# Kernel optimization log

Hardware: AMD Instinct MI355X
Metric: run time of the kernel (lower is better)

The kernel has to match this reference:

```python
import jax, jax.numpy as jnp
import numpy as np

N = 100000   # nodes
E = 1600000  # edges
IN = 128
H = 128
OUT = 128
G = 1000     # graphs


def setup_inputs() -> dict:
    key = jax.random.key(0)
    ks = jax.random.split(key, 6)
    x = jax.random.normal(ks[0], (N, IN), jnp.float32)
    edge_index = jax.random.randint(ks[1], (2, E), 0, N, dtype=jnp.int64)
    batch = jnp.sort(jax.random.randint(ks[2], (N,), 0, G, dtype=jnp.int64))
    # Glorot-ish init for the two GCN linear transforms
    W1 = jax.random.normal(ks[3], (IN, H), jnp.float32) * (1.0 / np.sqrt(IN))
    b1 = jnp.zeros((H,), jnp.float32)
    W2 = jax.random.normal(ks[4], (H, OUT), jnp.float32) * (1.0 / np.sqrt(H))
    b2 = jnp.zeros((OUT,), jnp.float32)
    return {"x": x, "edge_index": edge_index, "batch": batch,
            "W1": W1, "b1": b1, "W2": W2, "b2": b2, "num_graphs": G}


def reference(x, edge_index, batch, W1, b1, W2, b2, num_graphs):
    n = x.shape[0]
    src, dst = edge_index[0], edge_index[1]
    # GCN normalization with self-loops: deg includes the self-loop (+1)
    deg = jax.ops.segment_sum(jnp.ones(src.shape[0], x.dtype), dst,
                              num_segments=n) + 1.0
    dinv = jax.lax.rsqrt(deg)                 # [N]
    norm = dinv[src] * dinv[dst]              # [E] per-edge coefficient
    self_norm = dinv * dinv                   # [N] self-loop coefficient

    def gcn_conv(h, W, b):
        hw = h @ W                                            # [N, F] dense transform
        msg = norm[:, None] * hw[src]                         # gather + scale, [E, F]
        agg = jax.ops.segment_sum(msg, dst, num_segments=n)   # scatter-add
        return agg + self_norm[:, None] * hw + b              # self-loop + bias

    h = jax.nn.relu(gcn_conv(x, W1, b1))
    h = gcn_conv(h, W2, b2)

    # global_mean_pool over graph ids
    sums = jax.ops.segment_sum(h, batch, num_segments=num_graphs)
    counts = jax.ops.segment_sum(jnp.ones(n, h.dtype), batch,
                                 num_segments=num_graphs)
    return sums / jnp.maximum(counts, 1.0)[:, None]
```

## Files before the change

kernel.cpp:

```cpp
#include <hip/hip_runtime.h>
#include <hip/hip_fp16.h>

#define FDIM 128
#define BROWS 64
#define KCH 16
#define NCH (FDIM / KCH)
#define BSHIFT 9
#define BNODES 512
#define EPB 4096


__global__ __launch_bounds__(256) void bucket_count(const int* __restrict__ dst,
                                                    int* __restrict__ bcnt, int E) {
    __shared__ int lc[256];
    lc[threadIdx.x] = 0;
    __syncthreads();
    for (int e = blockIdx.x * blockDim.x + threadIdx.x; e < E;
         e += gridDim.x * blockDim.x)
        atomicAdd(&lc[dst[e] >> BSHIFT], 1);
    __syncthreads();
    int c = lc[threadIdx.x];
    if (c) atomicAdd(&bcnt[threadIdx.x], c);
}

__global__ void bucket_scan(const int* __restrict__ bcnt, int* __restrict__ bbase,
                            int* __restrict__ bcur, int* __restrict__ rp,
                            int E, int n, int nbuck) {
    __shared__ int s[2][256];
    int t = threadIdx.x;
    int v = (t < nbuck) ? bcnt[t] : 0;
    s[0][t] = v;
    __syncthreads();
    int cur = 0;
    for (int off = 1; off < 256; off <<= 1) {
        int x = s[cur][t];
        if (t >= off) x += s[cur][t - off];
        s[cur ^ 1][t] = x;
        cur ^= 1;
        __syncthreads();
    }
    int ex = s[cur][t] - v;
    if (t < nbuck) { bbase[t] = ex; bcur[t] = ex; }
    if (t == 0) { bbase[nbuck] = E; rp[n] = E; }
}

__global__ __launch_bounds__(256) void binscatter(const int* __restrict__ src,
                                                  const int* __restrict__ dst,
                                                  int* __restrict__ bcur,
                                                  unsigned* __restrict__ ebp, int E) {
    __shared__ int lcnt[256];
    __shared__ int gb[256];
    const int t = threadIdx.x;
    const int e0 = blockIdx.x * EPB;
    const int e1 = min(e0 + EPB, E);
    lcnt[t] = 0;
    __syncthreads();
    for (int e = e0 + t; e < e1; e += 256)
        atomicAdd(&lcnt[dst[e] >> BSHIFT], 1);
    __syncthreads();
    int c = lcnt[t];
    if (c) gb[t] = atomicAdd(&bcur[t], c);
    __syncthreads();
    lcnt[t] = 0;
    __syncthreads();
    for (int e = e0 + t; e < e1; e += 256) {
        int d = dst[e];
        int b = d >> BSHIFT;
        int lo = atomicAdd(&lcnt[b], 1);
        ebp[gb[b] + lo] = ((unsigned)src[e] << BSHIFT) | (unsigned)(d & (BNODES - 1));
    }
}

__global__ __launch_bounds__(256) void csr_build(const unsigned* __restrict__ ebp,
                                                 const int* __restrict__ bbase,
                                                 const int* __restrict__ batch,
                                                 int* __restrict__ rp,
                                                 float* __restrict__ dinv,
                                                 int* __restrict__ em,
                                                 int* __restrict__ gcnt, int n) {
    __shared__ int lcnt[BNODES];
    __shared__ int s[2][BNODES];
    __shared__ int lcur[BNODES];
    const int t = threadIdx.x;
    const int node0 = blockIdx.x << BSHIFT;
    const int nloc = min(BNODES, n - node0);
    lcnt[t] = 0; lcnt[t + 256] = 0;
    __syncthreads();
    const int eb0 = bbase[blockIdx.x], eb1 = bbase[blockIdx.x + 1];
    for (int e = eb0 + t; e < eb1; e += 256)
        atomicAdd(&lcnt[ebp[e] & (BNODES - 1)], 1);
    __syncthreads();
    s[0][t] = lcnt[t]; s[0][t + 256] = lcnt[t + 256];
    __syncthreads();
    int cur = 0;
    for (int off = 1; off < BNODES; off <<= 1) {
        int x0 = s[cur][t];       if (t >= off)       x0 += s[cur][t - off];
        int x1 = s[cur][t + 256]; if (t + 256 >= off) x1 += s[cur][t + 256 - off];
        s[cur ^ 1][t] = x0; s[cur ^ 1][t + 256] = x1;
        cur ^= 1;
        __syncthreads();
    }
    int ex0 = eb0 + s[cur][t] - lcnt[t];
    int ex1 = eb0 + s[cur][t + 256] - lcnt[t + 256];
    lcur[t] = ex0; lcur[t + 256] = ex1;
    if (t < nloc) {
        rp[node0 + t] = ex0;
        dinv[node0 + t] = rsqrtf((float)lcnt[t] + 1.0f);
    }
    if (t + 256 < nloc) {
        rp[node0 + t + 256] = ex1;
        dinv[node0 + t + 256] = rsqrtf((float)lcnt[t + 256] + 1.0f);
    }
    __syncthreads();
    for (int e = eb0 + t; e < eb1; e += 256) {
        unsigned v = ebp[e];
        int pos = atomicAdd(&lcur[v & (BNODES - 1)], 1);
        em[pos] = (int)(v >> BSHIFT);
    }
    if (t < nloc) atomicAdd(&gcnt[batch[node0 + t]], 1);
    if (t + 256 < nloc) atomicAdd(&gcnt[batch[node0 + t + 256]], 1);
}

__global__ __launch_bounds__(256) void gemm128(const float* __restrict__ X,
                                               const float* __restrict__ W,
                                               const float* __restrict__ dinv,
                                               __half* __restrict__ Y, int n) {
    __shared__ float Ws[FDIM * FDIM];
    __shared__ float xs[2][BROWS][KCH + 4];

    const int tid  = threadIdx.x;
    const int c    = tid & 15;
    const int r    = tid >> 4;
    const int srow = tid >> 2;
    const int skk  = (tid & 3) << 2;
    const int r0   = blockIdx.x * BROWS;

    for (int i = tid; i < FDIM * FDIM; i += 256) Ws[i] = W[i];

    const int grow  = r0 + srow;
    const bool rowok = grow < n;
    const float* xrow = X + (size_t)grow * FDIM + skk;

    float4 v = rowok ? *(const float4*)xrow : float4{0.f, 0.f, 0.f, 0.f};
    *(float4*)&xs[0][srow][skk] = v;
    __syncthreads();

    float accA[4][4], accB[4][4];
#pragma unroll
    for (int m = 0; m < 4; ++m)
#pragma unroll
        for (int i = 0; i < 4; ++i) { accA[m][i] = 0.f; accB[m][i] = 0.f; }

    for (int ch = 0; ch < NCH; ++ch) {
        const int b = ch & 1;
        float4 nv{0.f, 0.f, 0.f, 0.f};
        if (ch + 1 < NCH && rowok)
            nv = *(const float4*)(xrow + (ch + 1) * KCH);
        const int k0 = ch * KCH;
#pragma unroll
        for (int k4 = 0; k4 < KCH; k4 += 4) {
            float4 xv0 = *(const float4*)&xs[b][r][k4];
            float4 xv1 = *(const float4*)&xs[b][r + 16][k4];
            float4 xv2 = *(const float4*)&xs[b][r + 32][k4];
            float4 xv3 = *(const float4*)&xs[b][r + 48][k4];
#define GSTEP(kk, comp)                                                        \
            {                                                                  \
                const float* wp = &Ws[(k0 + k4 + kk) * FDIM + 4 * c];          \
                const float4 w0 = *(const float4*)wp;                          \
                const float4 w1 = *(const float4*)(wp + 64);                   \
                const float xr[4] = {xv0.comp, xv1.comp, xv2.comp, xv3.comp};  \
                _Pragma("unroll")                                              \
                for (int m = 0; m < 4; ++m) {                                  \
                    accA[m][0] = fmaf(xr[m], w0.x, accA[m][0]);                \
                    accA[m][1] = fmaf(xr[m], w0.y, accA[m][1]);                \
                    accA[m][2] = fmaf(xr[m], w0.z, accA[m][2]);                \
                    accB[m][0] = fmaf(xr[m], w1.x, accB[m][0]);                \
                    accB[m][1] = fmaf(xr[m], w1.y, accB[m][1]);                \
                    accB[m][2] = fmaf(xr[m], w1.z, accB[m][2]);                \
                    accB[m][3] = fmaf(xr[m], w1.w, accB[m][3]);                \
                    accA[m][3] = fmaf(xr[m], w0.w, accA[m][3]);                \
                }                                                              \
            }
            GSTEP(0, x) GSTEP(1, y) GSTEP(2, z) GSTEP(3, w)
#undef GSTEP
        }
        if (ch + 1 < NCH)
            *(float4*)&xs[b ^ 1][srow][skk] = nv;
        __syncthreads();
    }

#pragma unroll
    for (int m = 0; m < 4; ++m) {
        int row = r0 + r + 16 * m;
        if (row < n) {
            float dv = dinv[row];
            union { __half2 h[2]; uint2 u; } pa, pb;
            pa.h[0] = __floats2half2_rn(dv * accA[m][0], dv * accA[m][1]);
            pa.h[1] = __floats2half2_rn(dv * accA[m][2], dv * accA[m][3]);
            pb.h[0] = __floats2half2_rn(dv * accB[m][0], dv * accB[m][1]);
            pb.h[1] = __floats2half2_rn(dv * accB[m][2], dv * accB[m][3]);
            *(uint2*)&Y[(size_t)row * FDIM + 4 * c]      = pa.u;
            *(uint2*)&Y[(size_t)row * FDIM + 64 + 4 * c] = pb.u;
        }
    }
}

__device__ __forceinline__ void addv(float4& a, uint2 v) {
    __half2* h = (__half2*)&v;
    float2 f0 = __half22float2(h[0]);
    float2 f1 = __half22float2(h[1]);
    a.x += f0.x; a.y += f0.y; a.z += f1.x; a.w += f1.y;
}

__global__ __launch_bounds__(256) void aggregate_relu(
        const __half* __restrict__ hw, const int* __restrict__ rp,
        const int* __restrict__ em, const float* __restrict__ dinv,
        const float* __restrict__ bias, __half* __restrict__ out, int n) {
    const int lane = threadIdx.x & 31;
    const int node = blockIdx.x * 8 + (threadIdx.x >> 5);
    if (node >= n) return;
    const uint2* T = (const uint2*)hw;
    int e0 = rp[node], e1 = rp[node + 1];
    float4 a{0.f, 0.f, 0.f, 0.f};
    int e = e0;
    for (; e + 16 <= e1; e += 16) {
        uint2 v[16];
#pragma unroll
        for (int k = 0; k < 16; ++k) v[k] = T[(size_t)em[e + k] * 32 + lane];
#pragma unroll
        for (int k = 0; k < 16; ++k) addv(a, v[k]);
    }
    for (; e + 4 <= e1; e += 4) {
        uint2 v[4];
#pragma unroll
        for (int k = 0; k < 4; ++k) v[k] = T[(size_t)em[e + k] * 32 + lane];
#pragma unroll
        for (int k = 0; k < 4; ++k) addv(a, v[k]);
    }
    for (; e < e1; ++e) addv(a, T[(size_t)em[e] * 32 + lane]);
    addv(a, T[(size_t)node * 32 + lane]);
    float dv = dinv[node];
    float4 b = ((const float4*)bias)[lane];
    a.x = dv * fmaxf(fmaf(dv, a.x, b.x), 0.f);
    a.y = dv * fmaxf(fmaf(dv, a.y, b.y), 0.f);
    a.z = dv * fmaxf(fmaf(dv, a.z, b.z), 0.f);
    a.w = dv * fmaxf(fmaf(dv, a.w, b.w), 0.f);
    union { __half2 h[2]; uint2 u; } pk;
    pk.h[0] = __floats2half2_rn(a.x, a.y);
    pk.h[1] = __floats2half2_rn(a.z, a.w);
    ((uint2*)out)[(size_t)node * 32 + lane] = pk.u;
}

__global__ __launch_bounds__(256) void aggregate_pool(
        const __half* __restrict__ h1, const int* __restrict__ rp,
        const int* __restrict__ em, const float* __restrict__ dinv,
        const int* __restrict__ batch, float* __restrict__ pool, int n) {
    __shared__ float4 part[8][32];
    __shared__ int gs[8];
    const int lane = threadIdx.x & 31;
    const int half = threadIdx.x >> 5;
    const int node = blockIdx.x * 8 + half;
    const bool valid = node < n;
    const uint2* T = (const uint2*)h1;
    int e0 = 0, e1 = 0;
    if (valid) { e0 = rp[node]; e1 = rp[node + 1]; }
    float4 a{0.f, 0.f, 0.f, 0.f};
    int e = e0;
    for (; e + 16 <= e1; e += 16) {
        uint2 v[16];
#pragma unroll
        for (int k = 0; k < 16; ++k) v[k] = T[(size_t)em[e + k] * 32 + lane];
#pragma unroll
        for (int k = 0; k < 16; ++k) addv(a, v[k]);
    }
    for (; e + 4 <= e1; e += 4) {
        uint2 v[4];
#pragma unroll
        for (int k = 0; k < 4; ++k) v[k] = T[(size_t)em[e + k] * 32 + lane];
#pragma unroll
        for (int k = 0; k < 4; ++k) addv(a, v[k]);
    }
    for (; e < e1; ++e) addv(a, T[(size_t)em[e] * 32 + lane]);
    if (valid) {
        addv(a, T[(size_t)node * 32 + lane]);
        float dv = dinv[node];
        a.x *= dv; a.y *= dv; a.z *= dv; a.w *= dv;
    }
    part[half][lane] = a;
    if (lane == 0) gs[half] = valid ? batch[node] : -1;
    __syncthreads();
    if (half == 0) {
        float4 acc = part[0][lane];
        int g0 = gs[0];
#pragma unroll
        for (int h = 1; h < 8; ++h) {
            if (gs[h] == g0) {
                float4 p = part[h][lane];
                acc.x += p.x; acc.y += p.y; acc.z += p.z; acc.w += p.w;
            } else {
                if (g0 >= 0) {
                    float* dstp = &pool[g0 * FDIM + lane * 4];
                    atomicAdd(dstp + 0, acc.x); atomicAdd(dstp + 1, acc.y);
                    atomicAdd(dstp + 2, acc.z); atomicAdd(dstp + 3, acc.w);
                }
                g0 = gs[h];
                acc = part[h][lane];
            }
        }
        if (g0 >= 0) {
            float* dstp = &pool[g0 * FDIM + lane * 4];
            atomicAdd(dstp + 0, acc.x); atomicAdd(dstp + 1, acc.y);
            atomicAdd(dstp + 2, acc.z); atomicAdd(dstp + 3, acc.w);
        }
    }
}

__global__ __launch_bounds__(256) void pool_gemm(const float* __restrict__ pool,
                                                 const int* __restrict__ gcnt,
                                                 const float* __restrict__ W2,
                                                 const float* __restrict__ b2,
                                                 float* __restrict__ out, int G) {
    __shared__ float Ws[FDIM * FDIM];
    __shared__ float row[2][FDIM];
    for (int i = threadIdx.x; i < FDIM * FDIM; i += 256) Ws[i] = W2[i];
    const int j  = threadIdx.x & 127;
    const int gh = threadIdx.x >> 7;
    for (int g0 = blockIdx.x * 2; g0 < G; g0 += gridDim.x * 2) {
        const int g = g0 + gh;
        __syncthreads();
        int c = 0;
        if (g < G) {
            c = gcnt[g];
            float inv = (c > 0) ? 1.0f / (float)c : 0.0f;
            row[gh][j] = pool[g * FDIM + j] * inv;
        }
        __syncthreads();
        if (g < G) {
            float acc = (c > 0) ? b2[j] : 0.0f;
#pragma unroll
            for (int k = 0; k < FDIM; ++k)
                acc = fmaf(row[gh][k], Ws[k * FDIM + j], acc);
            out[g * FDIM + j] = acc;
        }
    }
}


extern "C" void kernel_launch(void* const* d_in, const int* in_sizes, int n_in,
                              void* d_out, int out_size, void* d_ws, size_t ws_size,
                              hipStream_t stream) {
    const float* x     = (const float*)d_in[0];
    const int*   ei    = (const int*)d_in[1];
    const int*   batch = (const int*)d_in[2];
    const float* W1    = (const float*)d_in[3];
    const float* b1    = (const float*)d_in[4];
    const float* W2    = (const float*)d_in[5];
    const float* b2    = (const float*)d_in[6];
    float* out = (float*)d_out;

    const int N = in_sizes[0] / FDIM;
    const int E = in_sizes[1] / 2;
    const int G = out_size / FDIM;
    const int* src = ei;
    const int* dst = ei + E;
    const int nbuck = (N + BNODES - 1) >> BSHIFT;

    char* p = (char*)d_ws;
    auto alloc = [&](size_t bytes) {
        void* r = (void*)p;
        p += (bytes + 255) & ~(size_t)255;
        return r;
    };
    float*    dinv  = (float*)   alloc((size_t)N * 4);
    int*      rp    = (int*)     alloc((size_t)(N + 1) * 4);
    int*      gcnt  = (int*)     alloc((size_t)G * 4);
    int*      bcnt  = (int*)     alloc(256 * 4);
    int*      bbase = (int*)     alloc(257 * 4);
    int*      bcur  = (int*)     alloc(256 * 4);
    unsigned* ebp   = (unsigned*)alloc((size_t)E * 4);
    int*      em    = (int*)     alloc((size_t)E * 4);
    __half*   hw    = (__half*)  alloc((size_t)N * FDIM * 2);
    __half*   h1    = (__half*)  alloc((size_t)N * FDIM * 2);
    float*    pool  = (float*)   alloc((size_t)G * FDIM * 4);

    hipMemsetAsync(bcnt, 0, 256 * 4, stream);
    hipMemsetAsync(gcnt, 0, (size_t)G * 4, stream);
    hipMemsetAsync(pool, 0, (size_t)G * FDIM * 4, stream);

    bucket_count<<<1024, 256, 0, stream>>>(dst, bcnt, E);
    bucket_scan<<<1, 256, 0, stream>>>(bcnt, bbase, bcur, rp, E, N, nbuck);
    binscatter<<<(E + EPB - 1) / EPB, 256, 0, stream>>>(src, dst, bcur, ebp, E);
    csr_build<<<nbuck, 256, 0, stream>>>(ebp, bbase, batch, rp, dinv, em, gcnt, N);

    const int GB = (N + BROWS - 1) / BROWS;
    gemm128<<<GB, 256, 0, stream>>>(x, W1, dinv, hw, N);
    aggregate_relu<<<(N + 7) / 8, 256, 0, stream>>>(hw, rp, em, dinv, b1, h1, N);
    aggregate_pool<<<(N + 7) / 8, 256, 0, stream>>>(h1, rp, em, dinv, batch, pool, N);
    pool_gemm<<<64, 256, 0, stream>>>(pool, gcnt, W2, b2, out, G);
}
```

Before: 410.0 us.

## Store features in sliced layout and aggregate per 16-feature slice

The GEMM now writes hw into eight feature-slice planes (16 halfs per node per slice), and the aggregation kernels give each block one slice for 64 nodes, with 4 lanes per node. The goal is a per-slice gather working set (about 3.2MB for 100k nodes) small enough to stay in cache, instead of random 256-byte row gathers over the full 25.6MB table. In exchange, the edge index array is read eight times, each gather is only a 32-byte access per node, and the pool reduction issues atomics per slice.

```diff
diff --git a/kernel.cpp b/kernel.cpp
--- a/kernel.cpp
+++ b/kernel.cpp
@@ -8,6 +8,8 @@
 #define BSHIFT 9
 #define BNODES 512
 #define EPB 4096
+#define NSLICE 8
+#define SFEAT 16
 
 
 __global__ __launch_bounds__(256) void bucket_count(const int* __restrict__ dst,
@@ -189,6 +191,7 @@
         __syncthreads();
     }
 
+    const size_t N4 = (size_t)n * 4;
 #pragma unroll
     for (int m = 0; m < 4; ++m) {
         int row = r0 + r + 16 * m;
@@ -199,8 +202,8 @@
             pa.h[1] = __floats2half2_rn(dv * accA[m][2], dv * accA[m][3]);
             pb.h[0] = __floats2half2_rn(dv * accB[m][0], dv * accB[m][1]);
             pb.h[1] = __floats2half2_rn(dv * accB[m][2], dv * accB[m][3]);
-            *(uint2*)&Y[(size_t)row * FDIM + 4 * c]      = pa.u;
-            *(uint2*)&Y[(size_t)row * FDIM + 64 + 4 * c] = pb.u;
+            ((uint2*)Y)[(size_t)(c >> 2) * N4 + (size_t)row * 4 + (c & 3)]       = pa.u;
+            ((uint2*)Y)[(size_t)(4 + (c >> 2)) * N4 + (size_t)row * 4 + (c & 3)] = pb.u;
         }
     }
 }
@@ -212,35 +215,33 @@
     a.x += f0.x; a.y += f0.y; a.z += f1.x; a.w += f1.y;
 }
 
-__global__ __launch_bounds__(256) void aggregate_relu(
+__global__ __launch_bounds__(256) void aggregate_relu_s(
         const __half* __restrict__ hw, const int* __restrict__ rp,
         const int* __restrict__ em, const float* __restrict__ dinv,
         const float* __restrict__ bias, __half* __restrict__ out, int n) {
-    const int lane = threadIdx.x & 31;
-    const int node = blockIdx.x * 8 + (threadIdx.x >> 5);
+    const int slice = blockIdx.x & (NSLICE - 1);
+    const int node0 = (blockIdx.x >> 3) * 64;
+    const int lane  = threadIdx.x & 63;
+    const int wave  = threadIdx.x >> 6;
+    const int group = lane >> 2;
+    const int sub   = lane & 3;
+    const int node  = node0 + wave * 16 + group;
     if (node >= n) return;
-    const uint2* T = (const uint2*)hw;
+    const uint2* Tb = (const uint2*)hw + (size_t)slice * n * 4;
     int e0 = rp[node], e1 = rp[node + 1];
     float4 a{0.f, 0.f, 0.f, 0.f};
     int e = e0;
-    for (; e + 16 <= e1; e += 16) {
-        uint2 v[16];
-#pragma unroll
-        for (int k = 0; k < 16; ++k) v[k] = T[(size_t)em[e + k] * 32 + lane];
-#pragma unroll
-        for (int k = 0; k < 16; ++k) addv(a, v[k]);
-    }
-    for (; e + 4 <= e1; e += 4) {
-        uint2 v[4];
-#pragma unroll
-        for (int k = 0; k < 4; ++k) v[k] = T[(size_t)em[e + k] * 32 + lane];
-#pragma unroll
-        for (int k = 0; k < 4; ++k) addv(a, v[k]);
-    }
-    for (; e < e1; ++e) addv(a, T[(size_t)em[e] * 32 + lane]);
-    addv(a, T[(size_t)node * 32 + lane]);
+    for (; e + 8 <= e1; e += 8) {
+        uint2 v[8];
+#pragma unroll
+        for (int k = 0; k < 8; ++k) v[k] = Tb[(size_t)em[e + k] * 4 + sub];
+#pragma unroll
+        for (int k = 0; k < 8; ++k) addv(a, v[k]);
+    }
+    for (; e < e1; ++e) addv(a, Tb[(size_t)em[e] * 4 + sub]);
+    addv(a, Tb[(size_t)node * 4 + sub]);
     float dv = dinv[node];
-    float4 b = ((const float4*)bias)[lane];
+    float4 b = ((const float4*)bias)[slice * 4 + sub];
     a.x = dv * fmaxf(fmaf(dv, a.x, b.x), 0.f);
     a.y = dv * fmaxf(fmaf(dv, a.y, b.y), 0.f);
     a.z = dv * fmaxf(fmaf(dv, a.z, b.z), 0.f);
@@ -248,69 +249,69 @@
     union { __half2 h[2]; uint2 u; } pk;
     pk.h[0] = __floats2half2_rn(a.x, a.y);
     pk.h[1] = __floats2half2_rn(a.z, a.w);
-    ((uint2*)out)[(size_t)node * 32 + lane] = pk.u;
-}
-
-__global__ __launch_bounds__(256) void aggregate_pool(
+    ((uint2*)out)[(size_t)slice * n * 4 + (size_t)node * 4 + sub] = pk.u;
+}
+
+__global__ __launch_bounds__(256) void aggregate_pool_s(
         const __half* __restrict__ h1, const int* __restrict__ rp,
         const int* __restrict__ em, const float* __restrict__ dinv,
         const int* __restrict__ batch, float* __restrict__ pool, int n) {
-    __shared__ float4 part[8][32];
-    __shared__ int gs[8];
-    const int lane = threadIdx.x & 31;
-    const int half = threadIdx.x >> 5;
-    const int node = blockIdx.x * 8 + half;
+    __shared__ float4 part[64][4];
+    __shared__ int gsh[64];
+    const int slice = blockIdx.x & (NSLICE - 1);
+    const int node0 = (blockIdx.x >> 3) * 64;
+    const int lane  = threadIdx.x & 63;
+    const int wave  = threadIdx.x >> 6;
+    const int group = lane >> 2;
+    const int sub   = lane & 3;
+    const int nl    = wave * 16 + group;
+    const int node  = node0 + nl;
     const bool valid = node < n;
-    const uint2* T = (const uint2*)h1;
+    const uint2* Tb = (const uint2*)h1 + (size_t)slice * n * 4;
     int e0 = 0, e1 = 0;
     if (valid) { e0 = rp[node]; e1 = rp[node + 1]; }
     float4 a{0.f, 0.f, 0.f, 0.f};
     int e = e0;
-    for (; e + 16 <= e1; e += 16) {
-        uint2 v[16];
-#pragma unroll
-        for (int k = 0; k < 16; ++k) v[k] = T[(size_t)em[e + k] * 32 + lane];
-#pragma unroll
-        for (int k = 0; k < 16; ++k) addv(a, v[k]);
-    }
-    for (; e + 4 <= e1; e += 4) {
-        uint2 v[4];
-#pragma unroll
-        for (int k = 0; k < 4; ++k) v[k] = T[(size_t)em[e + k] * 32 + lane];
-#pragma unroll
-        for (int k = 0; k < 4; ++k) addv(a, v[k]);
-    }
-    for (; e < e1; ++e) addv(a, T[(size_t)em[e] * 32 + lane]);
+    for (; e + 8 <= e1; e += 8) {
+        uint2 v[8];
+#pragma unroll
+        for (int k = 0; k < 8; ++k) v[k] = Tb[(size_t)em[e + k] * 4 + sub];
+#pragma unroll
+        for (int k = 0; k < 8; ++k) addv(a, v[k]);
+    }
+    for (; e < e1; ++e) addv(a, Tb[(size_t)em[e] * 4 + sub]);
     if (valid) {
-        addv(a, T[(size_t)node * 32 + lane]);
+        addv(a, Tb[(size_t)node * 4 + sub]);
         float dv = dinv[node];
         a.x *= dv; a.y *= dv; a.z *= dv; a.w *= dv;
     }
-    part[half][lane] = a;
-    if (lane == 0) gs[half] = valid ? batch[node] : -1;
-    __syncthreads();
-    if (half == 0) {
-        float4 acc = part[0][lane];
-        int g0 = gs[0];
-#pragma unroll
-        for (int h = 1; h < 8; ++h) {
-            if (gs[h] == g0) {
-                float4 p = part[h][lane];
-                acc.x += p.x; acc.y += p.y; acc.z += p.z; acc.w += p.w;
+    part[nl][sub] = a;
+    if (sub == 0) gsh[nl] = valid ? batch[node] : -1;
+    __syncthreads();
+    if (threadIdx.x < 16) {
+        const int msub = threadIdx.x & 3;
+        const int chunk = threadIdx.x >> 2;
+        float4 acc = part[chunk * 16][msub];
+        int g0 = gsh[chunk * 16];
+        for (int h = 1; h < 16; ++h) {
+            int gh = gsh[chunk * 16 + h];
+            float4 pv = part[chunk * 16 + h][msub];
+            if (gh == g0) {
+                acc.x += pv.x; acc.y += pv.y; acc.z += pv.z; acc.w += pv.w;
             } else {
                 if (g0 >= 0) {
-                    float* dstp = &pool[g0 * FDIM + lane * 4];
-                    atomicAdd(dstp + 0, acc.x); atomicAdd(dstp + 1, acc.y);
-                    atomicAdd(dstp + 2, acc.z); atomicAdd(dstp + 3, acc.w);
+                    float* dp = &pool[(size_t)g0 * FDIM + slice * SFEAT + msub * 4];
+                    atomicAdd(dp + 0, acc.x); atomicAdd(dp + 1, acc.y);
+                    atomicAdd(dp + 2, acc.z); atomicAdd(dp + 3, acc.w);
                 }
-                g0 = gs[h];
-                acc = part[h][lane];
+                g0 = gh;
+                acc = pv;
             }
         }
         if (g0 >= 0) {
-            float* dstp = &pool[g0 * FDIM + lane * 4];
-            atomicAdd(dstp + 0, acc.x); atomicAdd(dstp + 1, acc.y);
-            atomicAdd(dstp + 2, acc.z); atomicAdd(dstp + 3, acc.w);
+            float* dp = &pool[(size_t)g0 * FDIM + slice * SFEAT + msub * 4];
+            atomicAdd(dp + 0, acc.x); atomicAdd(dp + 1, acc.y);
+            atomicAdd(dp + 2, acc.z); atomicAdd(dp + 3, acc.w);
         }
     }
 }
@@ -393,8 +394,9 @@
     csr_build<<<nbuck, 256, 0, stream>>>(ebp, bbase, batch, rp, dinv, em, gcnt, N);
 
     const int GB = (N + BROWS - 1) / BROWS;
+    const int AB = ((N + 63) / 64) * NSLICE;
     gemm128<<<GB, 256, 0, stream>>>(x, W1, dinv, hw, N);
-    aggregate_relu<<<(N + 7) / 8, 256, 0, stream>>>(hw, rp, em, dinv, b1, h1, N);
-    aggregate_pool<<<(N + 7) / 8, 256, 0, stream>>>(h1, rp, em, dinv, batch, pool, N);
+    aggregate_relu_s<<<AB, 256, 0, stream>>>(hw, rp, em, dinv, b1, h1, N);
+    aggregate_pool_s<<<AB, 256, 0, stream>>>(h1, rp, em, dinv, batch, pool, N);
     pool_gemm<<<64, 256, 0, stream>>>(pool, gcnt, W2, b2, out, G);
 }
```

New measurement: 442.5 us. 7.9% more time.
